# Kernel tuning notes

Hardware: AMD Instinct MI355X
Metric: run time of the kernel (lower is better)

## Reference

```python
import jax, jax.numpy as jnp
import numpy as np

HEADS = 20  # head_dim = 1280 // 20 = 64
LORA_SCALE = 1.0


def setup_inputs() -> dict:
    key = jax.random.key(0)
    ks = jax.random.split(key, 16)
    B, S, C, R = 2, 2048, 1280, 4
    w = 0.02  # keep activations numerically tame
    inp = {
        "x": jax.random.normal(ks[0], (B, S, C), jnp.float32),
        "Wq": jax.random.normal(ks[1], (C, C), jnp.float32) * w,
        "Wk": jax.random.normal(ks[2], (C, C), jnp.float32) * w,
        "Wv": jax.random.normal(ks[3], (C, C), jnp.float32) * w,
        "Wo": jax.random.normal(ks[4], (C, C), jnp.float32) * w,
        "bo": jnp.zeros((C,), jnp.float32),
        "Aq": jax.random.normal(ks[5], (R, C), jnp.float32) * w,
        "Bq": jax.random.normal(ks[6], (C, R), jnp.float32) * w,
        "Ak": jax.random.normal(ks[7], (R, C), jnp.float32) * w,
        "Bk": jax.random.normal(ks[8], (C, R), jnp.float32) * w,
        "Av": jax.random.normal(ks[9], (R, C), jnp.float32) * w,
        "Bv": jax.random.normal(ks[10], (C, R), jnp.float32) * w,
        "Ao": jax.random.normal(ks[11], (R, C), jnp.float32) * w,
        "Bo": jax.random.normal(ks[12], (C, R), jnp.float32) * w,
    }
    return inp


def _lora(x, A, B):
    # LoRALinearLayer: up(down(x)); network_alpha=None -> no extra scaling
    return (x @ A.T) @ B.T


def reference(x, Wq, Wk, Wv, Wo, bo, Aq, Bq, Ak, Bk, Av, Bv, Ao, Bo):
    B, S, C = x.shape
    H = HEADS
    D = C // H
    # base projections + LoRA updates (self-attention: encoder_hidden_states = x)
    q = x @ Wq.T + LORA_SCALE * _lora(x, Aq, Bq)
    k = x @ Wk.T + LORA_SCALE * _lora(x, Ak, Bk)
    v = x @ Wv.T + LORA_SCALE * _lora(x, Av, Bv)
    # head split: [B, S, H, D]
    q = q.reshape(B, S, H, D)
    k = k.reshape(B, S, H, D)
    v = v.reshape(B, S, H, D)
    # explicit scores + softmax (attn.get_attention_scores), scale = 1/sqrt(D)
    scale = 1.0 / jnp.sqrt(jnp.asarray(D, x.dtype))
    scores = jnp.einsum("bshd,bthd->bhst", q, k) * scale  # [B, H, S, S]
    probs = jax.nn.softmax(scores, axis=-1)
    ctx = jnp.einsum("bhst,bthd->bshd", probs, v).reshape(B, S, C)
    # output projection (+bias) + LoRA; dropout is identity at eval
    out = ctx @ Wo.T + bo + LORA_SCALE * _lora(ctx, Ao, Bo)
    return out
```

## Files before the change

kernel.cpp:

```cpp
#include <hip/hip_runtime.h>

#define BATCH 2
#define SEQ   2048
#define CH    1280
#define NH    20
#define HD    64
#define BS    (BATCH*SEQ)
#define RK    4

typedef __attribute__((ext_vector_type(2)))  float floatx2;
typedef __attribute__((ext_vector_type(4)))  short bf16x4;
typedef __attribute__((ext_vector_type(8)))  short bf16x8;
typedef __attribute__((ext_vector_type(16))) float floatx16;

__device__ __forceinline__ floatx16 mfma32(bf16x8 a, bf16x8 b, floatx16 c) {
    return __builtin_amdgcn_mfma_f32_32x32x16_bf16(a, b, c, 0, 0, 0);
}
__device__ __forceinline__ floatx16 mfma32k8(bf16x4 a, bf16x4 b, floatx16 c) {
    return __builtin_amdgcn_mfma_f32_32x32x8bf16_1k(a, b, c, 0, 0, 0);
}

__device__ __forceinline__ unsigned short f2bf(float f) {
    unsigned int u = __float_as_uint(f);
    u += 0x7fffu + ((u >> 16) & 1u);
    return (unsigned short)(u >> 16);
}
__device__ __forceinline__ unsigned int packbf(float hi, float lo) {
    unsigned int a = __float_as_uint(hi) + 0x8000u;
    unsigned int b = __float_as_uint(lo) + 0x8000u;
    return __builtin_amdgcn_perm(a, b, 0x07060302u);
}
__device__ __forceinline__ float fexp2(float x) {
#if __has_builtin(__builtin_amdgcn_exp2f)
    return __builtin_amdgcn_exp2f(x);
#else
    return exp2f(x);
#endif
}

__device__ __forceinline__ void cp16(const unsigned short* g, unsigned short* l) {
    __builtin_amdgcn_global_load_lds(
        (const __attribute__((address_space(1))) unsigned int*)g,
        (__attribute__((address_space(3))) unsigned int*)l, 16, 0, 0);
}

__global__ __launch_bounds__(256) void fold_weights(
    const float* __restrict__ Wq, const float* __restrict__ Wk,
    const float* __restrict__ Wv, const float* __restrict__ Wo,
    const float* __restrict__ Aq, const float* __restrict__ Bq,
    const float* __restrict__ Ak, const float* __restrict__ Bk,
    const float* __restrict__ Av, const float* __restrict__ Bv,
    const float* __restrict__ Ao, const float* __restrict__ Bo,
    unsigned short* __restrict__ wq_bf, unsigned short* __restrict__ wk_bf,
    unsigned short* __restrict__ wv_bf, unsigned short* __restrict__ wo_bf)
{
    int e = blockIdx.x * 256 + threadIdx.x;
    int which = blockIdx.y;
    int i = e / CH, j = e % CH;
    const float *W, *A, *Bm;
    unsigned short* o;
    if (which == 0)      { W = Wq; A = Aq; Bm = Bq; o = wq_bf; }
    else if (which == 1) { W = Wk; A = Ak; Bm = Bk; o = wk_bf; }
    else if (which == 2) { W = Wv; A = Av; Bm = Bv; o = wv_bf; }
    else                 { W = Wo; A = Ao; Bm = Bo; o = wo_bf; }
    float acc = W[e];
#pragma unroll
    for (int r = 0; r < RK; r++) acc += Bm[i * RK + r] * A[r * CH + j];
    o[e] = f2bf(acc);
}

__global__ __launch_bounds__(256) void cast_x(const float* __restrict__ x,
                                              unsigned short* __restrict__ xb)
{
    int idx = (blockIdx.x * 256 + threadIdx.x) * 4;
    float4 v = *(const float4*)(x + idx);
    ushort4 o;
    o.x = f2bf(v.x); o.y = f2bf(v.y); o.z = f2bf(v.z); o.w = f2bf(v.w);
    *(ushort4*)(xb + idx) = o;
}

template<bool OUTF>
__device__ __forceinline__ void gemm128(
    const unsigned short* __restrict__ A, const unsigned short* __restrict__ B,
    unsigned short* __restrict__ obf, float* __restrict__ of,
    const float* __restrict__ bias, float oscale)
{
    __shared__ __align__(16) unsigned short sa[128 * 64];
    __shared__ __align__(16) unsigned short sb[128 * 64];
    const int tid = threadIdx.x;
    const int wav = tid >> 6, lane = tid & 63;
    const int n32 = lane & 31, half = lane >> 5;
    const int wr = wav >> 1, wc = wav & 1;
    const int M0 = blockIdx.y * 128, N0 = blockIdx.x * 128;

    const unsigned short* ga[4]; const unsigned short* gb[4];
    unsigned short* la[4]; unsigned short* lb[4];
#pragma unroll
    for (int g = 0; g < 4; g++) {
        int s = g * 256 + tid;
        int row = s >> 3, cc = (s & 7) ^ (row & 7);
        ga[g] = A + (size_t)(M0 + row) * CH + cc * 8;
        gb[g] = B + (size_t)(N0 + row) * CH + cc * 8;
        la[g] = sa + (size_t)(g * 256 + wav * 64) * 8;
        lb[g] = sb + (size_t)(g * 256 + wav * 64) * 8;
    }

    const int arow0 = wr * 64 + n32, brow0 = wc * 64 + n32;

    floatx16 acc[2][2];
#pragma unroll
    for (int mt = 0; mt < 2; mt++)
#pragma unroll
        for (int nt = 0; nt < 2; nt++)
#pragma unroll
            for (int r = 0; r < 16; r++) acc[mt][nt][r] = 0.f;

    for (int k0 = 0; k0 < CH; k0 += 64) {
#pragma unroll
        for (int g = 0; g < 4; g++) { cp16(ga[g], la[g]); cp16(gb[g], lb[g]); }
#pragma unroll
        for (int g = 0; g < 4; g++) { ga[g] += 64; gb[g] += 64; }
        __syncthreads();

        bf16x8 av[2][4], bv[2][4];
#pragma unroll
        for (int mt = 0; mt < 2; mt++) {
            const int ar = arow0 + mt * 32, br = brow0 + mt * 32;
#pragma unroll
            for (int ks = 0; ks < 4; ks++) {
                const int cc = ks * 2 + half;
                av[mt][ks] = *(const bf16x8*)(sa + ar * 64 + ((cc ^ (ar & 7)) << 3));
                bv[mt][ks] = *(const bf16x8*)(sb + br * 64 + ((cc ^ (br & 7)) << 3));
            }
        }
#pragma unroll
        for (int ks = 0; ks < 4; ks++)
#pragma unroll
            for (int mt = 0; mt < 2; mt++)
#pragma unroll
                for (int nt = 0; nt < 2; nt++)
                    acc[mt][nt] = mfma32(av[mt][ks], bv[nt][ks], acc[mt][nt]);
        __syncthreads();
    }

#pragma unroll
    for (int mt = 0; mt < 2; mt++) {
#pragma unroll
        for (int nt = 0; nt < 2; nt++) {
            const int col = N0 + wc * 64 + nt * 32 + n32;
            const float bv2 = OUTF ? bias[col] : 0.f;
#pragma unroll
            for (int r = 0; r < 16; r++) {
                size_t row = (size_t)(M0 + wr * 64 + mt * 32 +
                                      (r & 3) + 8 * (r >> 2) + 4 * half);
                if (OUTF) of[row * CH + col] = acc[mt][nt][r] + bv2;
                else      obf[row * CH + col] = f2bf(acc[mt][nt][r] * oscale);
            }
        }
    }
}

__global__ __launch_bounds__(256) void gemm_qkv(
    const unsigned short* __restrict__ xb,
    const unsigned short* __restrict__ wq, const unsigned short* __restrict__ wk,
    const unsigned short* __restrict__ wv,
    unsigned short* __restrict__ q, unsigned short* __restrict__ k,
    unsigned short* __restrict__ v)
{
    const unsigned short* w = blockIdx.z == 0 ? wq : blockIdx.z == 1 ? wk : wv;
    unsigned short* o = blockIdx.z == 0 ? q : blockIdx.z == 1 ? k : v;
    float scale = blockIdx.z == 0 ? 0.18033688011112042f : 1.0f;
    gemm128<false>(xb, w, o, nullptr, nullptr, scale);
}

__global__ __launch_bounds__(256) void gemm_o(
    const unsigned short* __restrict__ c_bf, const unsigned short* __restrict__ wo,
    const float* __restrict__ bias, float* __restrict__ out)
{
    gemm128<true>(c_bf, wo, nullptr, out, bias, 1.0f);
}

__global__ __launch_bounds__(256) void transpose_v(
    const unsigned short* __restrict__ v, unsigned short* __restrict__ vt)
{
    __shared__ unsigned short lds[32][34];
    const int s0 = blockIdx.x * 32;
    const int d0 = blockIdx.y * 32;
    const int bh = blockIdx.z, b = bh / NH, h = bh % NH;
    const int c = threadIdx.x & 31;
    const int rbase = threadIdx.x >> 5;
#pragma unroll
    for (int i = 0; i < 4; i++) {
        int r = rbase + i * 8;
        lds[r][c] = v[(size_t)(b * SEQ + s0 + r) * CH + h * HD + d0 + c];
    }
    __syncthreads();
    const int cperm = (c & ~12) | ((c & 4) << 1) | ((c & 8) >> 1);
#pragma unroll
    for (int i = 0; i < 4; i++) {
        int r = rbase + i * 8;
        vt[(size_t)(bh * HD + d0 + r) * SEQ + s0 + cperm] = lds[c][r];
    }
}

__global__ __launch_bounds__(256) void attention(
    const unsigned short* __restrict__ q, const unsigned short* __restrict__ k,
    const unsigned short* __restrict__ vt, unsigned short* __restrict__ c_bf)
{
    __shared__ __align__(16) unsigned short k_lds[128 * 64];
    __shared__ __align__(16) unsigned short v_lds[64 * 128];

    const int tid = threadIdx.x, wav = tid >> 6, lane = tid & 63;
    const int n32 = lane & 31, half = lane >> 5;
    const int q0 = blockIdx.x * 128;
    const int bh = blockIdx.y, b = bh / NH, h = bh % NH;

    const size_t qrow = (size_t)(b * SEQ + q0 + wav * 32 + n32);
    bf16x8 qf[4];
#pragma unroll
    for (int f = 0; f < 4; f++)
        qf[f] = *(const bf16x8*)(q + qrow * CH + h * HD + f * 16 + half * 8);

    const unsigned short* gk[4]; const unsigned short* gv[4];
    unsigned short* lk[4]; unsigned short* lv[4];
#pragma unroll
    for (int g = 0; g < 4; g++) {
        int s = g * 256 + tid;
        int rowk = s >> 3, cck = (s & 7) ^ (rowk & 7);
        gk[g] = k + (size_t)(b * SEQ + rowk) * CH + h * HD + cck * 8;
        lk[g] = k_lds + (size_t)(g * 256 + wav * 64) * 8;
        int rowv = s >> 4, ccv = (s & 15) ^ (rowv & 15);
        gv[g] = vt + (size_t)(bh * HD + rowv) * SEQ + ccv * 8;
        lv[g] = v_lds + (size_t)(g * 256 + wav * 64) * 8;
    }

    floatx2 ps = {0.f, 0.f};
    floatx16 acc[2];
#pragma unroll
    for (int dt = 0; dt < 2; dt++)
#pragma unroll
        for (int r = 0; r < 16; r++) acc[dt][r] = 0.f;

    for (int t0 = 0; t0 < SEQ; t0 += 128) {
#pragma unroll
        for (int g = 0; g < 4; g++) { cp16(gk[g], lk[g]); cp16(gv[g], lv[g]); }
#pragma unroll
        for (int g = 0; g < 4; g++) { gk[g] += (size_t)128 * CH; gv[g] += 128; }
        __syncthreads();

#pragma unroll
        for (int kt = 0; kt < 4; kt++) {
            const int keyrow = kt * 32 + n32;
            const unsigned short* kr = k_lds + keyrow * 64;
            floatx16 st;
#pragma unroll
            for (int r = 0; r < 16; r++) st[r] = 0.f;
#pragma unroll
            for (int f = 0; f < 4; f++) {
                int phys = (2 * f + half) ^ (keyrow & 7);
                bf16x8 kf = *(const bf16x8*)(kr + phys * 8);
                st = mfma32(kf, qf[f], st);
            }

            float p[16];
#pragma unroll
            for (int r = 0; r < 16; r++) p[r] = fexp2(st[r]);
            unsigned int pk[8];
#pragma unroll
            for (int j = 0; j < 8; j++) {
                ps += (floatx2){p[2 * j], p[2 * j + 1]};
                pk[j] = packbf(p[2 * j + 1], p[2 * j]);
            }

#pragma unroll
            for (int dt = 0; dt < 2; dt++) {
                const int drow = dt * 32 + n32;
                const unsigned short* vr = v_lds + drow * 128;
#pragma unroll
                for (int pp = 0; pp < 2; pp++) {
                    int ct = kt * 4 + pp * 2 + half;
                    int phys = ct ^ (drow & 15);
                    union { bf16x8 v8; bf16x4 v4[2]; } vv;
                    vv.v8 = *(const bf16x8*)(vr + phys * 8);
                    union { unsigned int u[2]; bf16x4 v; } pb0, pb1;
                    pb0.u[0] = pk[4 * pp + 0]; pb0.u[1] = pk[4 * pp + 1];
                    pb1.u[0] = pk[4 * pp + 2]; pb1.u[1] = pk[4 * pp + 3];
                    acc[dt] = mfma32k8(vv.v4[0], pb0.v, acc[dt]);
                    acc[dt] = mfma32k8(vv.v4[1], pb1.v, acc[dt]);
                }
            }
        }
        __syncthreads();
    }

    float psum = ps.x + ps.y;
    float tot = psum + __shfl_xor(psum, 32, 64);
    float rinv = __frcp_rn(tot);
    const size_t obase = qrow * CH + h * HD;
#pragma unroll
    for (int dt = 0; dt < 2; dt++) {
#pragma unroll
        for (int jj = 0; jj < 4; jj++) {
            int d = dt * 32 + 8 * jj + 4 * half;
            uint2 o2;
            o2.x = packbf(acc[dt][4 * jj + 1] * rinv, acc[dt][4 * jj + 0] * rinv);
            o2.y = packbf(acc[dt][4 * jj + 3] * rinv, acc[dt][4 * jj + 2] * rinv);
            *(uint2*)(c_bf + obase + d) = o2;
        }
    }
}

extern "C" void kernel_launch(void* const* d_in, const int* in_sizes, int n_in,
                              void* d_out, int out_size, void* d_ws, size_t ws_size,
                              hipStream_t stream)
{
    const float* x  = (const float*)d_in[0];
    const float* Wq = (const float*)d_in[1];
    const float* Wk = (const float*)d_in[2];
    const float* Wv = (const float*)d_in[3];
    const float* Wo = (const float*)d_in[4];
    const float* bo = (const float*)d_in[5];
    const float* Aq = (const float*)d_in[6];
    const float* Bq = (const float*)d_in[7];
    const float* Ak = (const float*)d_in[8];
    const float* Bk = (const float*)d_in[9];
    const float* Av = (const float*)d_in[10];
    const float* Bv = (const float*)d_in[11];
    const float* Ao = (const float*)d_in[12];
    const float* Bo = (const float*)d_in[13];
    float* out = (float*)d_out;

    char* ws = (char*)d_ws;
    size_t off = 0;
    auto alloc = [&](size_t bytes) -> void* {
        void* p = ws + off; off += (bytes + 255) & ~(size_t)255; return p;
    };
    const size_t WB = (size_t)CH * CH, XB = (size_t)BS * CH;
    unsigned short* wq_bf = (unsigned short*)alloc(WB * 2);
    unsigned short* wk_bf = (unsigned short*)alloc(WB * 2);
    unsigned short* wv_bf = (unsigned short*)alloc(WB * 2);
    unsigned short* wo_bf = (unsigned short*)alloc(WB * 2);
    unsigned short* x_bf  = (unsigned short*)alloc(XB * 2);
    unsigned short* q_bf  = (unsigned short*)alloc(XB * 2);
    unsigned short* k_bf  = (unsigned short*)alloc(XB * 2);
    unsigned short* v_bf  = (unsigned short*)alloc(XB * 2);
    unsigned short* vt_bf = (unsigned short*)alloc(XB * 2);
    unsigned short* c_bf  = (unsigned short*)alloc(XB * 2);
    (void)ws_size; (void)n_in; (void)in_sizes; (void)out_size;

    fold_weights<<<dim3(CH * CH / 256, 4), 256, 0, stream>>>(
        Wq, Wk, Wv, Wo, Aq, Bq, Ak, Bk, Av, Bv, Ao, Bo,
        wq_bf, wk_bf, wv_bf, wo_bf);

    cast_x<<<dim3(BS * CH / 1024), 256, 0, stream>>>(x, x_bf);

    gemm_qkv<<<dim3(CH / 128, BS / 128, 3), 256, 0, stream>>>(
        x_bf, wq_bf, wk_bf, wv_bf, q_bf, k_bf, v_bf);

    transpose_v<<<dim3(SEQ / 32, 2, BATCH * NH), 256, 0, stream>>>(v_bf, vt_bf);

    attention<<<dim3(SEQ / 128, BATCH * NH), 256, 0, stream>>>(
        q_bf, k_bf, vt_bf, c_bf);

    gemm_o<<<dim3(CH / 128, BS / 128), 256, 0, stream>>>(c_bf, wo_bf, bo, out);
}
```

Baseline: 289.7 us.

## Split attention key tiles across wave pairs and reduce partial outputs via LDS

Each attention block now covers 64 queries instead of 128, with two waves per query group each handling half of every 128-key tile. The partial accumulators and row sums are combined through LDS at the end. The grid doubles to 1280 blocks and launch bounds request 5 blocks per SM, to raise occupancy and latency hiding on the 256-CU device. In exchange, each K/V tile is loaded from global memory twice as often per query, and the end of the kernel gains an extra LDS reduction and barrier.

```diff
diff --git a/kernel.cpp b/kernel.cpp
--- a/kernel.cpp
+++ b/kernel.cpp
@@ -203,7 +203,7 @@
     }
 }
 
-__global__ __launch_bounds__(256) void attention(
+__global__ __launch_bounds__(256, 5) void attention(
     const unsigned short* __restrict__ q, const unsigned short* __restrict__ k,
     const unsigned short* __restrict__ vt, unsigned short* __restrict__ c_bf)
 {
@@ -212,27 +212,23 @@
 
     const int tid = threadIdx.x, wav = tid >> 6, lane = tid & 63;
     const int n32 = lane & 31, half = lane >> 5;
-    const int q0 = blockIdx.x * 128;
+    const int qw = wav & 1;
+    const int kh = wav >> 1;
+    const int q0 = blockIdx.x * 64;
     const int bh = blockIdx.y, b = bh / NH, h = bh % NH;
 
-    const size_t qrow = (size_t)(b * SEQ + q0 + wav * 32 + n32);
+    const size_t qrow = (size_t)(b * SEQ + q0 + qw * 32 + n32);
     bf16x8 qf[4];
 #pragma unroll
     for (int f = 0; f < 4; f++)
         qf[f] = *(const bf16x8*)(q + qrow * CH + h * HD + f * 16 + half * 8);
 
-    const unsigned short* gk[4]; const unsigned short* gv[4];
-    unsigned short* lk[4]; unsigned short* lv[4];
-#pragma unroll
-    for (int g = 0; g < 4; g++) {
-        int s = g * 256 + tid;
-        int rowk = s >> 3, cck = (s & 7) ^ (rowk & 7);
-        gk[g] = k + (size_t)(b * SEQ + rowk) * CH + h * HD + cck * 8;
-        lk[g] = k_lds + (size_t)(g * 256 + wav * 64) * 8;
-        int rowv = s >> 4, ccv = (s & 15) ^ (rowv & 15);
-        gv[g] = vt + (size_t)(bh * HD + rowv) * SEQ + ccv * 8;
-        lv[g] = v_lds + (size_t)(g * 256 + wav * 64) * 8;
-    }
+    const int rowk = tid >> 3, cck = (tid & 7) ^ (rowk & 7);
+    const int rowv = tid >> 4, ccv = (tid & 15) ^ (rowv & 15);
+    const unsigned short* gk0 = k + (size_t)(b * SEQ + rowk) * CH + h * HD + cck * 8;
+    const unsigned short* gv0 = vt + (size_t)(bh * HD + rowv) * SEQ + ccv * 8;
+    unsigned short* lk0 = k_lds + (size_t)(wav * 64) * 8;
+    unsigned short* lv0 = v_lds + (size_t)(wav * 64) * 8;
 
     floatx2 ps = {0.f, 0.f};
     floatx16 acc[2];
@@ -243,14 +239,16 @@
 
     for (int t0 = 0; t0 < SEQ; t0 += 128) {
 #pragma unroll
-        for (int g = 0; g < 4; g++) { cp16(gk[g], lk[g]); cp16(gv[g], lv[g]); }
-#pragma unroll
-        for (int g = 0; g < 4; g++) { gk[g] += (size_t)128 * CH; gv[g] += 128; }
+        for (int g = 0; g < 4; g++) {
+            cp16(gk0 + (size_t)g * 32 * CH, lk0 + g * 2048);
+            cp16(gv0 + g * 16 * SEQ, lv0 + g * 2048);
+        }
+        gk0 += (size_t)128 * CH; gv0 += 128;
         __syncthreads();
 
 #pragma unroll
-        for (int kt = 0; kt < 4; kt++) {
-            const int keyrow = kt * 32 + n32;
+        for (int kt = 0; kt < 2; kt++) {
+            const int keyrow = kh * 64 + kt * 32 + n32;
             const unsigned short* kr = k_lds + keyrow * 64;
             floatx16 st;
 #pragma unroll
@@ -278,7 +276,7 @@
                 const unsigned short* vr = v_lds + drow * 128;
 #pragma unroll
                 for (int pp = 0; pp < 2; pp++) {
-                    int ct = kt * 4 + pp * 2 + half;
+                    int ct = (kh * 2 + kt) * 4 + pp * 2 + half;
                     int phys = ct ^ (drow & 15);
                     union { bf16x8 v8; bf16x4 v4[2]; } vv;
                     vv.v8 = *(const bf16x8*)(vr + phys * 8);
@@ -295,17 +293,40 @@
 
     float psum = ps.x + ps.y;
     float tot = psum + __shfl_xor(psum, 32, 64);
-    float rinv = __frcp_rn(tot);
-    const size_t obase = qrow * CH + h * HD;
-#pragma unroll
-    for (int dt = 0; dt < 2; dt++) {
-#pragma unroll
-        for (int jj = 0; jj < 4; jj++) {
-            int d = dt * 32 + 8 * jj + 4 * half;
-            uint2 o2;
-            o2.x = packbf(acc[dt][4 * jj + 1] * rinv, acc[dt][4 * jj + 0] * rinv);
-            o2.y = packbf(acc[dt][4 * jj + 3] * rinv, acc[dt][4 * jj + 2] * rinv);
-            *(uint2*)(c_bf + obase + d) = o2;
+
+    float* facc = (float*)k_lds;
+    float* fps  = (float*)v_lds;
+    if (wav >= 2) {
+        const int wbase = (wav - 2) * 2048;
+#pragma unroll
+        for (int dt = 0; dt < 2; dt++)
+#pragma unroll
+            for (int r = 0; r < 16; r++)
+                facc[wbase + (dt * 16 + r) * 64 + lane] = acc[dt][r];
+        fps[(wav - 2) * 64 + lane] = tot;
+    }
+    __syncthreads();
+    if (wav < 2) {
+        const int wbase = wav * 2048;
+#pragma unroll
+        for (int dt = 0; dt < 2; dt++)
+#pragma unroll
+            for (int r = 0; r < 16; r++)
+                acc[dt][r] += facc[wbase + (dt * 16 + r) * 64 + lane];
+        tot += fps[wav * 64 + lane];
+
+        float rinv = __frcp_rn(tot);
+        const size_t obase = qrow * CH + h * HD;
+#pragma unroll
+        for (int dt = 0; dt < 2; dt++) {
+#pragma unroll
+            for (int jj = 0; jj < 4; jj++) {
+                int d = dt * 32 + 8 * jj + 4 * half;
+                uint2 o2;
+                o2.x = packbf(acc[dt][4 * jj + 1] * rinv, acc[dt][4 * jj + 0] * rinv);
+                o2.y = packbf(acc[dt][4 * jj + 3] * rinv, acc[dt][4 * jj + 2] * rinv);
+                *(uint2*)(c_bf + obase + d) = o2;
+            }
         }
     }
 }
@@ -359,7 +380,7 @@
 
     transpose_v<<<dim3(SEQ / 32, 2, BATCH * NH), 256, 0, stream>>>(v_bf, vt_bf);
 
-    attention<<<dim3(SEQ / 128, BATCH * NH), 256, 0, stream>>>(
+    attention<<<dim3(SEQ / 64, BATCH * NH), 256, 0, stream>>>(
         q_bf, k_bf, vt_bf, c_bf);
 
     gemm_o<<<dim3(CH / 128, BS / 128), 256, 0, stream>>>(c_bf, wo_bf, bo, out);
```

After: 287.4 us. No clear change (-0.8%).
